# Kernel optimization log

Measured on AMD Instinct MI355X. Metric: run time of the kernel, lower is better.

Reference implementation:

```python
import jax, jax.numpy as jnp
import numpy as np

EMBED = 1024
HEADS = 16
HEAD_DIM = EMBED // HEADS
FFN = 4 * EMBED
EPS = 1e-5


def _layernorm(x, g, b):
    mu = jnp.mean(x, axis=-1, keepdims=True)
    var = jnp.mean(jnp.square(x - mu), axis=-1, keepdims=True)
    return (x - mu) * jax.lax.rsqrt(var + EPS) * g + b


def setup_inputs() -> dict:
    key = jax.random.key(0)
    ks = jax.random.split(key, 12)
    s = lambda fan_in: 1.0 / np.sqrt(fan_in)
    return {
        "x": jax.random.normal(ks[0], (4, 2048, EMBED), dtype=jnp.float32),
        # per-head_dim projections (shared across heads), stored [in, out]
        "Wq": jax.random.uniform(ks[1], (HEAD_DIM, HEAD_DIM), jnp.float32, -s(HEAD_DIM), s(HEAD_DIM)),
        "Wk": jax.random.uniform(ks[2], (HEAD_DIM, HEAD_DIM), jnp.float32, -s(HEAD_DIM), s(HEAD_DIM)),
        "Wv": jax.random.uniform(ks[3], (HEAD_DIM, HEAD_DIM), jnp.float32, -s(HEAD_DIM), s(HEAD_DIM)),
        "Wo": jax.random.uniform(ks[4], (EMBED, EMBED), jnp.float32, -s(EMBED), s(EMBED)),
        "bo": jax.random.uniform(ks[5], (EMBED,), jnp.float32, -s(EMBED), s(EMBED)),
        "ln1_g": jnp.ones((EMBED,), jnp.float32),
        "ln1_b": jnp.zeros((EMBED,), jnp.float32),
        "ln2_g": jnp.ones((EMBED,), jnp.float32),
        "ln2_b": jnp.zeros((EMBED,), jnp.float32),
        "W1": jax.random.uniform(ks[6], (EMBED, FFN), jnp.float32, -s(EMBED), s(EMBED)),
        "b1": jax.random.uniform(ks[7], (FFN,), jnp.float32, -s(EMBED), s(EMBED)),
        "W2": jax.random.uniform(ks[8], (FFN, EMBED), jnp.float32, -s(FFN), s(FFN)),
        "b2": jax.random.uniform(ks[9], (EMBED,), jnp.float32, -s(FFN), s(FFN)),
    }


def reference(x, Wq, Wk, Wv, Wo, bo, ln1_g, ln1_b, ln2_g, ln2_b, W1, b1, W2, b2):
    N, S, E = x.shape
    xn = _layernorm(x, ln1_g, ln1_b)                      # pre-LN
    h = xn.reshape(N, S, HEADS, HEAD_DIM)                 # [N,S,H,D]
    q = jnp.einsum('nshd,de->nshe', h, Wq)
    k = jnp.einsum('nshd,de->nshe', h, Wk)
    v = jnp.einsum('nshd,de->nshe', h, Wv)
    # note: original scales by sqrt(embed_size), not sqrt(head_dim)
    energy = jnp.einsum('nqhd,nkhd->nhqk', q, k) / jnp.sqrt(jnp.asarray(E, x.dtype))
    attn = jax.nn.softmax(energy, axis=-1)                # [N,H,S,S]
    ctx = jnp.einsum('nhqk,nkhd->nqhd', attn, v).reshape(N, S, E)
    attn_out = x + (ctx @ Wo + bo)                        # residual 1
    an = _layernorm(attn_out, ln2_g, ln2_b)
    ff = jax.nn.gelu(an @ W1 + b1, approximate=False) @ W2 + b2
    return attn_out + ff                                  # residual 2
```

## Files before the change

### kernel.cpp

```cpp
#include <hip/hip_runtime.h>
#include <hip/hip_bf16.h>
#include <cstdint>
#include <math.h>

#define EMBED 1024
#define HEADS 16
#define HDIM 64
#define SEQ 2048
#define TOKENS 8192

typedef __attribute__((ext_vector_type(8))) short short8;
typedef __attribute__((ext_vector_type(4))) float f32x4;
typedef unsigned short ushort_t;

__device__ __forceinline__ float bf2f(ushort_t u) {
  union { unsigned int i; float f; } c; c.i = ((unsigned int)u) << 16; return c.f;
}
__device__ __forceinline__ ushort_t f2bf(float f) {
  union { float f; unsigned int i; } c; c.f = f;
  unsigned int x = c.i;
  unsigned int r = x + 0x7fffu + ((x >> 16) & 1u);
  return (ushort_t)(r >> 16);
}
__device__ __forceinline__ void g2lds16(const void* g, void* l) {
  __builtin_amdgcn_global_load_lds(
      (const __attribute__((address_space(1))) unsigned int*)g,
      (__attribute__((address_space(3))) unsigned int*)l, 16, 0, 0);
}

__global__ __launch_bounds__(256) void transpose_cast_k(const float* __restrict__ in,
                                                        ushort_t* __restrict__ out,
                                                        int R, int C) {
  __shared__ ushort_t tile[32][33];
  int tx = threadIdx.x & 31, ty = threadIdx.x >> 5;
  int c0 = blockIdx.x * 32, r0 = blockIdx.y * 32;
#pragma unroll
  for (int i = ty; i < 32; i += 8)
    tile[i][tx] = f2bf(in[(long)(r0 + i) * C + (c0 + tx)]);
  __syncthreads();
#pragma unroll
  for (int i = ty; i < 32; i += 8) out[(long)(c0 + i) * R + (r0 + tx)] = tile[tx][i];
}

__global__ __launch_bounds__(256) void ln_k(const float* __restrict__ xin,
                                            const float* __restrict__ g,
                                            const float* __restrict__ b,
                                            ushort_t* __restrict__ out) {
  int row = blockIdx.x, t = threadIdx.x;
  long base = (long)row * EMBED + t * 4;
  f32x4 xv = *(const f32x4*)(xin + base);
  float v[4] = {xv[0], xv[1], xv[2], xv[3]};
  float s1 = v[0] + v[1] + v[2] + v[3];
  float s2 = v[0]*v[0] + v[1]*v[1] + v[2]*v[2] + v[3]*v[3];
#pragma unroll
  for (int m = 1; m < 64; m <<= 1) { s1 += __shfl_xor(s1, m, 64); s2 += __shfl_xor(s2, m, 64); }
  __shared__ float ws1[4], ws2[4];
  int w = t >> 6, lane = t & 63;
  if (lane == 0) { ws1[w] = s1; ws2[w] = s2; }
  __syncthreads();
  float S1 = ws1[0] + ws1[1] + ws1[2] + ws1[3];
  float S2 = ws2[0] + ws2[1] + ws2[2] + ws2[3];
  float mean = S1 * (1.0f / EMBED);
  float var = S2 * (1.0f / EMBED) - mean * mean;
  float rstd = rsqrtf(var + 1e-5f);
#pragma unroll
  for (int j = 0; j < 4; ++j) {
    int c = t * 4 + j;
    out[(long)row * EMBED + c] = f2bf((v[j] - mean) * rstd * g[c] + b[c]);
  }
}

__global__ __launch_bounds__(256) void qkv_k(const ushort_t* __restrict__ xn,
                                             const ushort_t* __restrict__ WqT,
                                             const ushort_t* __restrict__ WkT,
                                             const ushort_t* __restrict__ WvT,
                                             ushort_t* __restrict__ q, ushort_t* __restrict__ k,
                                             ushort_t* __restrict__ v) {
  __shared__ __align__(16) ushort_t As[128 * 64];
  int t = threadIdx.x;
  long rowbase = (long)blockIdx.x * 128;
#pragma unroll
  for (int p = 0; p < 4; ++p) {
    int idx = p * 256 + t;
    int row = idx >> 3, chunk = idx & 7;
    g2lds16(xn + (rowbase + row) * 64 + chunk * 8, As + idx * 8);
  }
  __syncthreads();
  int w = t >> 6, lane = t & 63, l15 = lane & 15, quad = lane >> 4;
  short8 af[2][2];
#pragma unroll
  for (int mi = 0; mi < 2; ++mi)
#pragma unroll
    for (int ks = 0; ks < 2; ++ks)
      af[mi][ks] = *(const short8*)(As + (w * 32 + mi * 16 + l15) * 64 + ks * 32 + quad * 8);
  const ushort_t* Ws[3] = {WqT, WkT, WvT};
  ushort_t* Os[3] = {q, k, v};
#pragma unroll
  for (int wsel = 0; wsel < 3; ++wsel) {
    const ushort_t* W = Ws[wsel];
    short8 bfr[4][2];
#pragma unroll
    for (int ni = 0; ni < 4; ++ni)
#pragma unroll
      for (int ks = 0; ks < 2; ++ks)
        bfr[ni][ks] = *(const short8*)(W + (ni * 16 + l15) * 64 + ks * 32 + quad * 8);
    f32x4 acc[2][4] = {};
#pragma unroll
    for (int mi = 0; mi < 2; ++mi)
#pragma unroll
      for (int ni = 0; ni < 4; ++ni)
#pragma unroll
        for (int ks = 0; ks < 2; ++ks)
          acc[mi][ni] = __builtin_amdgcn_mfma_f32_16x16x32_bf16(af[mi][ks], bfr[ni][ks],
                                                                acc[mi][ni], 0, 0, 0);
    ushort_t* O = Os[wsel];
#pragma unroll
    for (int mi = 0; mi < 2; ++mi)
#pragma unroll
      for (int ni = 0; ni < 4; ++ni)
#pragma unroll
        for (int r = 0; r < 4; ++r) {
          long rg = rowbase + w * 32 + mi * 16 + quad * 4 + r;
          O[rg * 64 + ni * 16 + l15] = f2bf(acc[mi][ni][r]);
        }
  }
}

#define KSTR 72
__global__ __launch_bounds__(256) void attn_k(const ushort_t* __restrict__ q,
                                              const ushort_t* __restrict__ kk,
                                              const ushort_t* __restrict__ vv,
                                              ushort_t* __restrict__ ctx) {
  __shared__ __align__(16) ushort_t sm[64 * KSTR * 2 + 4 * 16 * KSTR];
  ushort_t* Ks = sm;
  ushort_t* Vt = sm + 64 * KSTR;
  ushort_t* Ps = sm + 128 * KSTR;
  int t = threadIdx.x;
  int qt = blockIdx.x, bh = blockIdx.y;
  int n = bh >> 4, h = bh & 15;
  long qtok0 = (long)n * SEQ + qt * 64;
  int w = t >> 6, lane = t & 63, l15 = lane & 15, quad = lane >> 4;
  short8 qf[2];
#pragma unroll
  for (int ks = 0; ks < 2; ++ks)
    qf[ks] = *(const short8*)(q + (qtok0 + w * 16 + l15) * EMBED + h * HDIM + ks * 32 + quad * 8);
  float m_run[4] = {-1e30f, -1e30f, -1e30f, -1e30f};
  float l_run[4] = {0.f, 0.f, 0.f, 0.f};
  f32x4 acc_o[4] = {};
  const float sc = 1.0f / 32.0f;
  for (int kt = 0; kt < SEQ / 64; ++kt) {
    long ktok0 = (long)n * SEQ + kt * 64;
    short8 kreg[2];
#pragma unroll
    for (int p = 0; p < 2; ++p) {
      int idx = p * 256 + t;
      int key = idx >> 3, chunk = idx & 7;
      kreg[p] = *(const short8*)(kk + (ktok0 + key) * EMBED + h * HDIM + chunk * 8);
    }
    short8 vreg[2];
#pragma unroll
    for (int p = 0; p < 2; ++p) {
      int idx = p * 256 + t;
      int key = idx & 63, c = idx >> 6;
      vreg[p] = *(const short8*)(vv + (ktok0 + key) * EMBED + h * HDIM + c * 8);
    }
    __syncthreads();
#pragma unroll
    for (int p = 0; p < 2; ++p) {
      int idx = p * 256 + t;
      int key = idx >> 3, chunk = idx & 7;
      *(short8*)(Ks + key * KSTR + chunk * 8) = kreg[p];
    }
#pragma unroll
    for (int p = 0; p < 2; ++p) {
      int idx = p * 256 + t;
      int key = idx & 63, c = idx >> 6;
#pragma unroll
      for (int j = 0; j < 8; ++j) Vt[(c * 8 + j) * KSTR + key] = (ushort_t)vreg[p][j];
    }
    __syncthreads();
    f32x4 s[4] = {};
#pragma unroll
    for (int ks = 0; ks < 2; ++ks) {
#pragma unroll
      for (int nf = 0; nf < 4; ++nf) {
        short8 bb = *(const short8*)(Ks + (nf * 16 + l15) * KSTR + ks * 32 + quad * 8);
        s[nf] = __builtin_amdgcn_mfma_f32_16x16x32_bf16(qf[ks], bb, s[nf], 0, 0, 0);
      }
    }
#pragma unroll
    for (int nf = 0; nf < 4; ++nf)
#pragma unroll
      for (int j = 0; j < 4; ++j) s[nf][j] *= sc;
    float mnew[4], alpha[4];
#pragma unroll
    for (int j = 0; j < 4; ++j) {
      float m = fmaxf(fmaxf(s[0][j], s[1][j]), fmaxf(s[2][j], s[3][j]));
#pragma unroll
      for (int d = 1; d < 16; d <<= 1) m = fmaxf(m, __shfl_xor(m, d, 64));
      mnew[j] = fmaxf(m_run[j], m);
      alpha[j] = __expf(m_run[j] - mnew[j]);
      m_run[j] = mnew[j];
    }
    float rsum[4] = {0.f, 0.f, 0.f, 0.f};
#pragma unroll
    for (int nf = 0; nf < 4; ++nf)
#pragma unroll
      for (int j = 0; j < 4; ++j) {
        float p = __expf(s[nf][j] - mnew[j]);
        s[nf][j] = p;
        rsum[j] += p;
      }
#pragma unroll
    for (int j = 0; j < 4; ++j) {
      float r = rsum[j];
#pragma unroll
      for (int d = 1; d < 16; d <<= 1) r += __shfl_xor(r, d, 64);
      l_run[j] = l_run[j] * alpha[j] + r;
    }
#pragma unroll
    for (int nf = 0; nf < 4; ++nf)
#pragma unroll
      for (int j = 0; j < 4; ++j) acc_o[nf][j] *= alpha[j];
    ushort_t* Pw = Ps + w * 16 * KSTR;
#pragma unroll
    for (int nf = 0; nf < 4; ++nf)
#pragma unroll
      for (int j = 0; j < 4; ++j)
        Pw[(quad * 4 + j) * KSTR + nf * 16 + l15] = f2bf(s[nf][j]);
#pragma unroll
    for (int ks = 0; ks < 2; ++ks) {
      short8 a = *(const short8*)(Pw + l15 * KSTR + ks * 32 + quad * 8);
#pragma unroll
      for (int nf = 0; nf < 4; ++nf) {
        short8 bb = *(const short8*)(Vt + (nf * 16 + l15) * KSTR + ks * 32 + quad * 8);
        acc_o[nf] = __builtin_amdgcn_mfma_f32_16x16x32_bf16(a, bb, acc_o[nf], 0, 0, 0);
      }
    }
  }
#pragma unroll
  for (int nf = 0; nf < 4; ++nf)
#pragma unroll
    for (int j = 0; j < 4; ++j) {
      long tok = qtok0 + w * 16 + quad * 4 + j;
      float inv_l = 1.0f / fmaxf(l_run[j], 1e-30f);
      ctx[(tok * HEADS + h) * HDIM + nf * 16 + l15] = f2bf(acc_o[nf][j] * inv_l);
    }
}

__global__ __launch_bounds__(256) void gemm_bt(const ushort_t* __restrict__ A,
                                               const ushort_t* __restrict__ BT,
                                               const float* __restrict__ bias,
                                               const float* __restrict__ res,
                                               ushort_t* __restrict__ out_bf,
                                               float* __restrict__ out_f,
                                               int M, int N, int K, int mode) {
  __shared__ __align__(16) ushort_t As[128 * 32];
  __shared__ __align__(16) ushort_t Bs[128 * 32];
  int t = threadIdx.x;
  long m0 = (long)blockIdx.y * 128;
  long n0 = (long)blockIdx.x * 128;
  int w = t >> 6, lane = t & 63, l15 = lane & 15, quad = lane >> 4;
  int wm = w >> 1, wn = w & 1;
  f32x4 acc[4][4] = {};
  for (int kt = 0; kt < K; kt += 32) {
    __syncthreads();
#pragma unroll
    for (int p = 0; p < 2; ++p) {
      int idx = p * 256 + t;
      int row = idx >> 2, chunk = idx & 3;
      g2lds16(A + (m0 + row) * K + kt + chunk * 8, As + idx * 8);
      g2lds16(BT + (n0 + row) * K + kt + chunk * 8, Bs + idx * 8);
    }
    __syncthreads();
    short8 af[4], bfr[4];
#pragma unroll
    for (int mi = 0; mi < 4; ++mi)
      af[mi] = *(const short8*)(As + (wm * 64 + mi * 16 + l15) * 32 + quad * 8);
#pragma unroll
    for (int ni = 0; ni < 4; ++ni)
      bfr[ni] = *(const short8*)(Bs + (wn * 64 + ni * 16 + l15) * 32 + quad * 8);
#pragma unroll
    for (int mi = 0; mi < 4; ++mi)
#pragma unroll
      for (int ni = 0; ni < 4; ++ni)
        acc[mi][ni] = __builtin_amdgcn_mfma_f32_16x16x32_bf16(af[mi], bfr[ni], acc[mi][ni], 0, 0, 0);
  }
#pragma unroll
  for (int mi = 0; mi < 4; ++mi)
#pragma unroll
    for (int ni = 0; ni < 4; ++ni) {
      long col = n0 + wn * 64 + ni * 16 + l15;
      float bv = bias[col];
#pragma unroll
      for (int r = 0; r < 4; ++r) {
        long row = m0 + wm * 64 + mi * 16 + quad * 4 + r;
        long off = row * N + col;
        float val = acc[mi][ni][r] + bv;
        if (mode == 0) {
          out_f[off] = val + res[off];
        } else if (mode == 1) {
          val = 0.5f * val * (1.0f + erff(val * 0.70710678118654752f));
          out_bf[off] = f2bf(val);
        } else {
          out_f[off] = val + res[off];
        }
      }
    }
}

extern "C" void kernel_launch(void* const* d_in, const int* in_sizes, int n_in,
                              void* d_out, int out_size, void* d_ws, size_t ws_size,
                              hipStream_t stream) {
  (void)in_sizes; (void)n_in; (void)out_size; (void)ws_size;
  const float* x   = (const float*)d_in[0];
  const float* Wq  = (const float*)d_in[1];
  const float* Wk  = (const float*)d_in[2];
  const float* Wv  = (const float*)d_in[3];
  const float* Wo  = (const float*)d_in[4];
  const float* bo  = (const float*)d_in[5];
  const float* l1g = (const float*)d_in[6];
  const float* l1b = (const float*)d_in[7];
  const float* l2g = (const float*)d_in[8];
  const float* l2b = (const float*)d_in[9];
  const float* W1  = (const float*)d_in[10];
  const float* b1  = (const float*)d_in[11];
  const float* W2  = (const float*)d_in[12];
  const float* b2  = (const float*)d_in[13];
  float* out = (float*)d_out;

  char* ws = (char*)d_ws;
  const size_t MB = 1ull << 20;
  ushort_t* XN  = (ushort_t*)(ws);
  ushort_t* Q   = (ushort_t*)(ws + 16 * MB);
  ushort_t* Kb  = (ushort_t*)(ws + 32 * MB);
  ushort_t* Vb  = (ushort_t*)(ws + 48 * MB);
  float*    AO  = (float*)(ws + 64 * MB);
  ushort_t* CTX = XN;
  ushort_t* AN  = (ushort_t*)(ws + 96 * MB);
  ushort_t* FF1 = (ushort_t*)(ws);
  ushort_t* WoT = (ushort_t*)(ws + 112 * MB);
  ushort_t* W1T = (ushort_t*)(ws + 114 * MB);
  ushort_t* W2T = (ushort_t*)(ws + 122 * MB);
  ushort_t* WqT = (ushort_t*)(ws + 130 * MB);
  ushort_t* WkT = WqT + 4096;
  ushort_t* WvT = WkT + 4096;

  dim3 b256(256);
  transpose_cast_k<<<dim3(2, 2), b256, 0, stream>>>(Wq, WqT, 64, 64);
  transpose_cast_k<<<dim3(2, 2), b256, 0, stream>>>(Wk, WkT, 64, 64);
  transpose_cast_k<<<dim3(2, 2), b256, 0, stream>>>(Wv, WvT, 64, 64);
  transpose_cast_k<<<dim3(32, 32), b256, 0, stream>>>(Wo, WoT, 1024, 1024);
  transpose_cast_k<<<dim3(128, 32), b256, 0, stream>>>(W1, W1T, 1024, 4096);
  transpose_cast_k<<<dim3(32, 128), b256, 0, stream>>>(W2, W2T, 4096, 1024);

  ln_k<<<dim3(TOKENS), b256, 0, stream>>>(x, l1g, l1b, XN);
  qkv_k<<<dim3(1024), b256, 0, stream>>>(XN, WqT, WkT, WvT, Q, Kb, Vb);
  attn_k<<<dim3(32, 64), b256, 0, stream>>>(Q, Kb, Vb, CTX);
  gemm_bt<<<dim3(8, 64), b256, 0, stream>>>(CTX, WoT, bo, x, nullptr, AO,
                                            TOKENS, EMBED, EMBED, 0);
  ln_k<<<dim3(TOKENS), b256, 0, stream>>>(AO, l2g, l2b, AN);
  gemm_bt<<<dim3(32, 64), b256, 0, stream>>>(AN, W1T, b1, nullptr, FF1, nullptr,
                                             TOKENS, 4096, EMBED, 1);
  gemm_bt<<<dim3(8, 64), b256, 0, stream>>>(FF1, W2T, b2, AO, nullptr, out,
                                            TOKENS, EMBED, 4096, 2);
}
```

Baseline: 724.1 us.

## Compute transposed scores in attention to keep P in registers, drop LDS roundtrip

The attention kernel now computes S^T = K·Q^T, so each lane holds one query's scores. The softmax max and sum then need only two cross-lane shuffles, and P can be packed straight into the MFMA B operand without staging through LDS. V is written to LDS in a permuted column order so it matches the register layout of P. The 1/32 softmax scale moves into the Q projection epilogue, and outputs are written as packed bf16 pairs using cheaper round-half-up rounding. The rounding change slightly alters numerics, and correctness depends on the permutation matching the MFMA layout.

```diff
diff --git a/kernel.cpp b/kernel.cpp
--- a/kernel.cpp
+++ b/kernel.cpp
@@ -21,6 +21,11 @@
   unsigned int x = c.i;
   unsigned int r = x + 0x7fffu + ((x >> 16) & 1u);
   return (ushort_t)(r >> 16);
+}
+__device__ __forceinline__ unsigned int pack_bf16_rhu(float a, float b) {
+  unsigned int ua = __float_as_uint(a) + 0x8000u;
+  unsigned int ub = __float_as_uint(b) + 0x8000u;
+  return __builtin_amdgcn_perm(ub, ua, 0x07060302u);
 }
 __device__ __forceinline__ void g2lds16(const void* g, void* l) {
   __builtin_amdgcn_global_load_lds(
@@ -98,6 +103,7 @@
 #pragma unroll
   for (int wsel = 0; wsel < 3; ++wsel) {
     const ushort_t* W = Ws[wsel];
+    float oscale = (wsel == 0) ? 0.03125f : 1.0f;
     short8 bfr[4][2];
 #pragma unroll
     for (int ni = 0; ni < 4; ++ni)
@@ -121,7 +127,7 @@
 #pragma unroll
         for (int r = 0; r < 4; ++r) {
           long rg = rowbase + w * 32 + mi * 16 + quad * 4 + r;
-          O[rg * 64 + ni * 16 + l15] = f2bf(acc[mi][ni][r]);
+          O[rg * 64 + ni * 16 + l15] = f2bf(acc[mi][ni][r] * oscale);
         }
   }
 }
@@ -131,10 +137,9 @@
                                               const ushort_t* __restrict__ kk,
                                               const ushort_t* __restrict__ vv,
                                               ushort_t* __restrict__ ctx) {
-  __shared__ __align__(16) ushort_t sm[64 * KSTR * 2 + 4 * 16 * KSTR];
+  __shared__ __align__(16) ushort_t sm[64 * KSTR * 2];
   ushort_t* Ks = sm;
   ushort_t* Vt = sm + 64 * KSTR;
-  ushort_t* Ps = sm + 128 * KSTR;
   int t = threadIdx.x;
   int qt = blockIdx.x, bh = blockIdx.y;
   int n = bh >> 4, h = bh & 15;
@@ -144,10 +149,10 @@
 #pragma unroll
   for (int ks = 0; ks < 2; ++ks)
     qf[ks] = *(const short8*)(q + (qtok0 + w * 16 + l15) * EMBED + h * HDIM + ks * 32 + quad * 8);
-  float m_run[4] = {-1e30f, -1e30f, -1e30f, -1e30f};
-  float l_run[4] = {0.f, 0.f, 0.f, 0.f};
+  int vkey = t & 63;
+  int vcol = (vkey & 32) | ((vkey & 12) << 1) | ((vkey & 16) >> 2) | (vkey & 3);
+  float m_run = -1e30f, l_run = 0.f;
   f32x4 acc_o[4] = {};
-  const float sc = 1.0f / 32.0f;
   for (int kt = 0; kt < SEQ / 64; ++kt) {
     long ktok0 = (long)n * SEQ + kt * 64;
     short8 kreg[2];
@@ -160,9 +165,8 @@
     short8 vreg[2];
 #pragma unroll
     for (int p = 0; p < 2; ++p) {
-      int idx = p * 256 + t;
-      int key = idx & 63, c = idx >> 6;
-      vreg[p] = *(const short8*)(vv + (ktok0 + key) * EMBED + h * HDIM + c * 8);
+      int c = p * 4 + (t >> 6);
+      vreg[p] = *(const short8*)(vv + (ktok0 + vkey) * EMBED + h * HDIM + c * 8);
     }
     __syncthreads();
 #pragma unroll
@@ -173,79 +177,76 @@
     }
 #pragma unroll
     for (int p = 0; p < 2; ++p) {
-      int idx = p * 256 + t;
-      int key = idx & 63, c = idx >> 6;
-#pragma unroll
-      for (int j = 0; j < 8; ++j) Vt[(c * 8 + j) * KSTR + key] = (ushort_t)vreg[p][j];
+      int c = p * 4 + (t >> 6);
+#pragma unroll
+      for (int j = 0; j < 8; ++j) Vt[(c * 8 + j) * KSTR + vcol] = (ushort_t)vreg[p][j];
     }
     __syncthreads();
-    f32x4 s[4] = {};
+    f32x4 st[4] = {};
 #pragma unroll
     for (int ks = 0; ks < 2; ++ks) {
 #pragma unroll
       for (int nf = 0; nf < 4; ++nf) {
-        short8 bb = *(const short8*)(Ks + (nf * 16 + l15) * KSTR + ks * 32 + quad * 8);
-        s[nf] = __builtin_amdgcn_mfma_f32_16x16x32_bf16(qf[ks], bb, s[nf], 0, 0, 0);
+        short8 kf = *(const short8*)(Ks + (nf * 16 + l15) * KSTR + ks * 32 + quad * 8);
+        st[nf] = __builtin_amdgcn_mfma_f32_16x16x32_bf16(kf, qf[ks], st[nf], 0, 0, 0);
       }
     }
+    float mx = st[0][0];
 #pragma unroll
     for (int nf = 0; nf < 4; ++nf)
 #pragma unroll
-      for (int j = 0; j < 4; ++j) s[nf][j] *= sc;
-    float mnew[4], alpha[4];
-#pragma unroll
-    for (int j = 0; j < 4; ++j) {
-      float m = fmaxf(fmaxf(s[0][j], s[1][j]), fmaxf(s[2][j], s[3][j]));
-#pragma unroll
-      for (int d = 1; d < 16; d <<= 1) m = fmaxf(m, __shfl_xor(m, d, 64));
-      mnew[j] = fmaxf(m_run[j], m);
-      alpha[j] = __expf(m_run[j] - mnew[j]);
-      m_run[j] = mnew[j];
-    }
-    float rsum[4] = {0.f, 0.f, 0.f, 0.f};
+      for (int r = 0; r < 4; ++r) mx = fmaxf(mx, st[nf][r]);
+    mx = fmaxf(mx, __shfl_xor(mx, 16, 64));
+    mx = fmaxf(mx, __shfl_xor(mx, 32, 64));
+    float mnew = fmaxf(m_run, mx);
+    float alpha = __expf(m_run - mnew);
+    m_run = mnew;
+    float rsum = 0.f;
 #pragma unroll
     for (int nf = 0; nf < 4; ++nf)
 #pragma unroll
-      for (int j = 0; j < 4; ++j) {
-        float p = __expf(s[nf][j] - mnew[j]);
-        s[nf][j] = p;
-        rsum[j] += p;
+      for (int r = 0; r < 4; ++r) {
+        float pv = __expf(st[nf][r] - mnew);
+        st[nf][r] = pv;
+        rsum += pv;
       }
-#pragma unroll
-    for (int j = 0; j < 4; ++j) {
-      float r = rsum[j];
-#pragma unroll
-      for (int d = 1; d < 16; d <<= 1) r += __shfl_xor(r, d, 64);
-      l_run[j] = l_run[j] * alpha[j] + r;
-    }
+    rsum += __shfl_xor(rsum, 16, 64);
+    rsum += __shfl_xor(rsum, 32, 64);
+    l_run = l_run * alpha + rsum;
 #pragma unroll
     for (int nf = 0; nf < 4; ++nf)
 #pragma unroll
-      for (int j = 0; j < 4; ++j) acc_o[nf][j] *= alpha[j];
-    ushort_t* Pw = Ps + w * 16 * KSTR;
+      for (int r = 0; r < 4; ++r) acc_o[nf][r] *= alpha;
+    unsigned int Dk[4][2];
 #pragma unroll
     for (int nf = 0; nf < 4; ++nf)
 #pragma unroll
-      for (int j = 0; j < 4; ++j)
-        Pw[(quad * 4 + j) * KSTR + nf * 16 + l15] = f2bf(s[nf][j]);
+      for (int hh = 0; hh < 2; ++hh)
+        Dk[nf][hh] = pack_bf16_rhu(st[nf][2 * hh], st[nf][2 * hh + 1]);
 #pragma unroll
     for (int ks = 0; ks < 2; ++ks) {
-      short8 a = *(const short8*)(Pw + l15 * KSTR + ks * 32 + quad * 8);
+      union { unsigned int u[4]; short8 s8; } pf;
+      pf.u[0] = Dk[2 * ks][0];
+      pf.u[1] = Dk[2 * ks][1];
+      pf.u[2] = Dk[2 * ks + 1][0];
+      pf.u[3] = Dk[2 * ks + 1][1];
 #pragma unroll
       for (int nf = 0; nf < 4; ++nf) {
-        short8 bb = *(const short8*)(Vt + (nf * 16 + l15) * KSTR + ks * 32 + quad * 8);
-        acc_o[nf] = __builtin_amdgcn_mfma_f32_16x16x32_bf16(a, bb, acc_o[nf], 0, 0, 0);
+        short8 vf = *(const short8*)(Vt + (nf * 16 + l15) * KSTR + ks * 32 + quad * 8);
+        acc_o[nf] = __builtin_amdgcn_mfma_f32_16x16x32_bf16(vf, pf.s8, acc_o[nf], 0, 0, 0);
       }
     }
   }
-#pragma unroll
-  for (int nf = 0; nf < 4; ++nf)
-#pragma unroll
-    for (int j = 0; j < 4; ++j) {
-      long tok = qtok0 + w * 16 + quad * 4 + j;
-      float inv_l = 1.0f / fmaxf(l_run[j], 1e-30f);
-      ctx[(tok * HEADS + h) * HDIM + nf * 16 + l15] = f2bf(acc_o[nf][j] * inv_l);
-    }
+  float inv_l = 1.0f / fmaxf(l_run, 1e-30f);
+  long tok = qtok0 + w * 16 + l15;
+#pragma unroll
+  for (int nf = 0; nf < 4; ++nf) {
+    unsigned int d0 = pack_bf16_rhu(acc_o[nf][0] * inv_l, acc_o[nf][1] * inv_l);
+    unsigned int d1 = pack_bf16_rhu(acc_o[nf][2] * inv_l, acc_o[nf][3] * inv_l);
+    unsigned int* dst = (unsigned int*)(ctx + tok * EMBED + h * HDIM + nf * 16 + quad * 4);
+    dst[0] = d0;
+    dst[1] = d1;
+  }
 }
 
 __global__ __launch_bounds__(256) void gemm_bt(const ushort_t* __restrict__ A,
```

New measurement: 622.1 us. -14.1%, faster.
